# Performance work log

Measured on AMD Instinct MI355X. Metric: run time of the kernel, lower is better.

The kernel has to match this reference:

```python
import jax, jax.numpy as jnp
import numpy as np

RATE = 0.999  # moving_average_rate
EPS_NORM = 1e-12
EPS_CNT = 1e-6


def l2norm(v, axis=-1):
    # matches torch F.normalize(dim=axis) with default eps
    n = jnp.sqrt(jnp.sum(v * v, axis=axis, keepdims=True))
    return v / jnp.maximum(n, EPS_NORM)


def setup_inputs() -> dict:
    key = jax.random.key(0)
    ks = jax.random.split(key, 7)
    b, c, h, w, k = 8, 256, 64, 64, 2048
    x = jax.random.normal(ks[0], (b, c, h, w), dtype=jnp.float32)
    y = jax.random.uniform(ks[1], (b, 4, h, w), dtype=jnp.float32)
    feat_w = jax.random.normal(ks[2], (k, c + 4), dtype=jnp.float32) * 0.02
    w1 = jax.random.normal(ks[3], (c + 4, c), dtype=jnp.float32) * 0.02
    b1 = jnp.zeros((c,), dtype=jnp.float32)
    w2 = jax.random.normal(ks[4], (c, c), dtype=jnp.float32) * 0.02
    b2 = jnp.zeros((c,), dtype=jnp.float32)
    return {"x": x, "y": y, "feat_w": feat_w, "w1": w1, "b1": b1, "w2": w2, "b2": b2}


def reference(x, y, feat_w, w1, b1, w2, b2):
    b, c, h, w = x.shape
    k = feat_w.shape[0]
    # flatten spatial: (n, c) with n = b*h*w
    x_flat = jnp.transpose(x, (0, 2, 3, 1)).reshape(-1, c)
    y_flat = jnp.transpose(y, (0, 2, 3, 1)).reshape(-1, 4)

    # cosine-similarity scores against codebook features (no grad in original)
    xn = l2norm(x_flat)                       # (n, c)
    mn = l2norm(feat_w[:, :-4])               # (k, c)
    score = xn @ mn.T                         # (n, k)

    # top1 EMA codebook update
    xy = jnp.concatenate([x_flat, y_flat], axis=1)          # (n, c+4)
    ind = jnp.argmax(score, axis=1)                          # (n,)
    counts = jax.ops.segment_sum(jnp.ones_like(ind, jnp.float32), ind, num_segments=k)  # (k,)
    sums = jax.ops.segment_sum(xy, ind, num_segments=k)      # (k, c+4)
    embed_mean = sums / (counts[:, None] + EPS_CNT)          # (k, c+4)
    new_w = feat_w * RATE + embed_mean * (1.0 - RATE)        # (k, c+4)

    # softmax attention over (updated) normalized codebook
    p = jax.nn.softmax(score, axis=1)                        # (n, k)
    out = p @ l2norm(new_w)                                  # (n, c+4)

    # MLP: Linear -> GELU -> Linear (drop=0)
    out = jax.nn.gelu(out @ w1 + b1) @ w2 + b2               # (n, c)
    return jnp.transpose(out.reshape(b, h, w, c), (0, 3, 1, 2))
```

## Files before the change

kernel.cpp:

```cpp
#include <hip/hip_runtime.h>
#include <cstdint>
#include <cstddef>


typedef short v8s __attribute__((ext_vector_type(8)));
typedef float v4f __attribute__((ext_vector_type(4)));

__device__ __forceinline__ unsigned short f2b(float f) {
  unsigned u = __float_as_uint(f);
  u = (u + 0x7FFFu + ((u >> 16) & 1u)) >> 16;
  return (unsigned short)u;
}
__device__ __forceinline__ float b2f(short s) {
  return __uint_as_float((unsigned)(unsigned short)s << 16);
}
__device__ __forceinline__ float gelu_t(float x) {
  float x3 = x * x * x;
  return 0.5f * x * (1.0f + tanhf(0.7978845608028654f * (x + 0.044715f * x3)));
}
__device__ __forceinline__ float gelu_fast(float x) {
  float u = 0.7978845608028654f * (x + 0.044715f * x * x * x);
  float tt = __expf(2.0f * u);
  return x * tt * __builtin_amdgcn_rcpf(tt + 1.0f);
}
__device__ __forceinline__ unsigned int mono(float f) {
  unsigned u = __float_as_uint(f);
  return (u & 0x80000000u) ? ~u : (u | 0x80000000u);
}
__device__ __forceinline__ void async16(const short* g, short* l) {
  __builtin_amdgcn_global_load_lds(
      (const __attribute__((address_space(1))) unsigned int*)g,
      (__attribute__((address_space(3))) unsigned int*)l, 16, 0, 0);
}

__global__ void transpose_norm_kernel(const float* __restrict__ x, short* __restrict__ xn,
                                      float* __restrict__ norms) {
  __shared__ float tile[32 * 257];
  __shared__ float part[8][32];
  __shared__ float invn[32];
  int t = threadIdx.x, bx = blockIdx.x;
  int b = bx >> 7, st = bx & 127;
  int s0 = st * 32;
  int sl = t & 31, cp = t >> 5;
  const float* xb = x + (size_t)b * 256 * 4096 + s0 + sl;
  float ss = 0.f;
#pragma unroll 4
  for (int i = 0; i < 32; ++i) {
    int c = cp * 32 + i;
    float v = xb[(size_t)c * 4096];
    tile[sl * 257 + c] = v;
    ss += v * v;
  }
  part[cp][sl] = ss;
  __syncthreads();
  if (t < 32) {
    float tot = 0.f;
#pragma unroll
    for (int p = 0; p < 8; ++p) tot += part[p][t];
    float nrm = fmaxf(sqrtf(tot), 1e-12f);
    invn[t] = 1.0f / nrm;
    norms[(size_t)b * 4096 + s0 + t] = nrm;
  }
  __syncthreads();
  size_t obase = ((size_t)b * 4096 + s0) * 256 + t;
  for (int s = 0; s < 32; ++s)
    xn[obase + (size_t)s * 256] = (short)f2b(tile[s * 257 + t] * invn[s]);
}

__global__ void cbnorm_kernel(const float* __restrict__ fw, short* __restrict__ mn) {
  int t = threadIdx.x;
  int wv = t >> 6, l = t & 63;
  int r = blockIdx.x * 4 + wv;
  const float* row = fw + (size_t)r * 260;
  float v[4]; float ss = 0.f;
#pragma unroll
  for (int p = 0; p < 4; ++p) { v[p] = row[l + p * 64]; ss += v[p] * v[p]; }
#pragma unroll
  for (int m = 1; m < 64; m <<= 1) ss += __shfl_xor(ss, m, 64);
  float inv = 1.0f / fmaxf(sqrtf(ss), 1e-12f);
#pragma unroll
  for (int p = 0; p < 4; ++p) mn[(size_t)r * 256 + l + p * 64] = (short)f2b(v[p] * inv);
}

template <int KTOT, int LDA, int LDB>
__device__ __forceinline__ void gemm_core(const short* __restrict__ A, const short* __restrict__ B,
                                          int mt, int nt, int t, v4f acc[4][4],
                                          short* As, short* Bs) {
  const int l = t & 63, w = t >> 6;
  const int wm = w >> 1, wn = w & 1;
  const int lane16 = l & 15, q4 = l >> 4;
#pragma unroll
  for (int i = 0; i < 4; ++i)
#pragma unroll
    for (int j = 0; j < 4; ++j)
#pragma unroll
      for (int r = 0; r < 4; ++r) acc[i][j][r] = 0.0f;
  const int srow = (w << 5) + (l >> 2);
  const int scol = (l & 3) << 3;
  const short* ga = A + (size_t)(mt * 128 + srow) * LDA + scol;
  const short* gb = B + (size_t)(nt * 128 + srow) * LDB + scol;
  short* la = As + (w << 5) * 32;
  short* lb = Bs + (w << 5) * 32;
  for (int kk = 0; kk < KTOT; kk += 32) {
    async16(ga + kk, la);
    async16(ga + (size_t)16 * LDA + kk, la + 16 * 32);
    async16(gb + kk, lb);
    async16(gb + (size_t)16 * LDB + kk, lb + 16 * 32);
    __syncthreads();
    v8s af[4], bf[4];
#pragma unroll
    for (int i = 0; i < 4; ++i) af[i] = *(const v8s*)&As[(wm * 64 + i * 16 + lane16) * 32 + q4 * 8];
#pragma unroll
    for (int j = 0; j < 4; ++j) bf[j] = *(const v8s*)&Bs[(wn * 64 + j * 16 + lane16) * 32 + q4 * 8];
#pragma unroll
    for (int i = 0; i < 4; ++i)
#pragma unroll
      for (int j = 0; j < 4; ++j)
        acc[i][j] = __builtin_amdgcn_mfma_f32_16x16x32_bf16(af[i], bf[j], acc[i][j], 0, 0, 0);
    __syncthreads();
  }
}

__global__ __launch_bounds__(256, 2) void gemm1_kernel(const short* __restrict__ A, const short* __restrict__ B,
                                                       short* __restrict__ Q,
                                                       unsigned long long* __restrict__ packed,
                                                       float* __restrict__ lrow) {
  __shared__ __align__(16) short As[128 * 32];
  __shared__ __align__(16) short Bs[128 * 32];
  int t = threadIdx.x, bx = blockIdx.x;
  int mt = bx >> 4, nt = bx & 15;
  v4f acc[4][4];
  gemm_core<256, 256, 256>(A, B, mt, nt, t, acc, As, Bs);
  int l = t & 63, w = t >> 6, wm = w >> 1, wn = w & 1, lane16 = l & 15, q4 = l >> 4;
  int rowbase = mt * 128 + wm * 64, colbase = nt * 128 + wn * 64;
#pragma unroll
  for (int i = 0; i < 4; ++i) {
#pragma unroll
    for (int r = 0; r < 4; ++r) {
      int row_g = rowbase + i * 16 + q4 * 4 + r;
      float qs = 0.f;
      unsigned long long best = 0ull;
#pragma unroll
      for (int j = 0; j < 4; ++j) {
        float s = acc[i][j][r];
        int col_g = colbase + j * 16 + lane16;
        float qv = __expf(s) - 1.0f;
        Q[(size_t)row_g * 2048 + col_g] = (short)f2b(qv);
        qs += qv;
        unsigned long long key = ((unsigned long long)mono(s) << 32) |
                                 (unsigned long long)(unsigned int)(~(unsigned)col_g);
        if (key > best) best = key;
      }
#pragma unroll
      for (int m = 1; m < 16; m <<= 1) {
        unsigned long long ob = __shfl_xor(best, m, 64);
        if (ob > best) best = ob;
        qs += __shfl_xor(qs, m, 64);
      }
      if (lane16 == 0) {
        atomicMax(&packed[row_g], best);
        atomicAdd(&lrow[row_g], qs);
      }
    }
  }
}

__global__ void ind_kernel(const unsigned long long* __restrict__ packed,
                           int* __restrict__ ind, float* __restrict__ cnt) {
  int i = blockIdx.x * 256 + threadIdx.x;
  unsigned int lowbits = (unsigned int)(packed[i] & 0xFFFFFFFFull);
  int id = (int)(~lowbits);
  ind[i] = id;
  atomicAdd(&cnt[id], 1.0f);
}

__global__ void scan_kernel(const float* __restrict__ cnt, int* __restrict__ offs,
                            int* __restrict__ cursor) {
  __shared__ int part[256];
  int t = threadIdx.x;
  int local[8]; int s = 0;
#pragma unroll
  for (int i = 0; i < 8; ++i) { local[i] = s; s += (int)cnt[t * 8 + i]; }
  part[t] = s;
  __syncthreads();
  for (int off = 1; off < 256; off <<= 1) {
    int v = (t >= off) ? part[t - off] : 0;
    __syncthreads();
    part[t] += v;
    __syncthreads();
  }
  int base = (t > 0) ? part[t - 1] : 0;
#pragma unroll
  for (int i = 0; i < 8; ++i) {
    int o = base + local[i];
    offs[t * 8 + i] = o;
    cursor[t * 8 + i] = o;
  }
  if (t == 255) offs[2048] = part[255];
}

__global__ void fill_kernel(const int* __restrict__ ind, int* __restrict__ cursor,
                            int* __restrict__ sorted) {
  int i = blockIdx.x * 256 + threadIdx.x;
  int id = ind[i];
  int pos = atomicAdd(&cursor[id], 1);
  sorted[pos] = i;
}

__global__ void segsum_kernel(const short* __restrict__ xn, const float* __restrict__ norms,
                              const float* __restrict__ y, const int* __restrict__ offs,
                              const int* __restrict__ sorted, float* __restrict__ sums) {
  int r = blockIdx.x, t = threadIdx.x;
  int beg = offs[r], end = offs[r + 1];
  float a0 = 0.f, a1 = 0.f;
  for (int j = beg; j < end; ++j) {
    int node = sorted[j];
    float nm = norms[node];
    a0 += b2f(xn[(size_t)node * 256 + t]) * nm;
    if (t < 4) {
      int b = node >> 12, s = node & 4095;
      a1 += y[(size_t)b * 16384 + t * 4096 + s];
    }
  }
  sums[(size_t)r * 260 + t] = a0;
  if (t < 4) sums[(size_t)r * 260 + 256 + t] = a1;
}

__global__ void neww_kernel(const float* __restrict__ fw, const float* __restrict__ sums,
                            const float* __restrict__ cnt, short* __restrict__ nwt,
                            float* __restrict__ colsum) {
  int r = blockIdx.x;
  int l = threadIdx.x;
  float cv = cnt[r] + 1e-6f;
  float vals[5]; float ss = 0.f;
#pragma unroll
  for (int p = 0; p < 5; ++p) {
    int c = l + p * 64;
    float v = 0.f;
    if (c < 260) {
      float m = sums[(size_t)r * 260 + c] / cv;
      v = fw[(size_t)r * 260 + c] * 0.999f + m * 0.001f;
    }
    vals[p] = v; ss += v * v;
  }
#pragma unroll
  for (int m = 1; m < 64; m <<= 1) ss += __shfl_xor(ss, m, 64);
  float inv = 1.0f / fmaxf(sqrtf(ss), 1e-12f);
#pragma unroll
  for (int p = 0; p < 5; ++p) {
    int c = l + p * 64;
    if (c < 260) {
      float v = vals[p] * inv;
      nwt[(size_t)c * 2048 + r] = (short)f2b(v);
      atomicAdd(&colsum[c], v);
    }
  }
}

__global__ void const_kernel(const float* __restrict__ colsum, const float* __restrict__ w1,
                             const float* __restrict__ b1, const float* __restrict__ w2,
                             const float* __restrict__ b2, float* __restrict__ c0,
                             float* __restrict__ zc, float* __restrict__ hc,
                             float* __restrict__ oc) {
  __shared__ float c0s[260], hcs[256];
  int t = threadIdx.x;
  for (int c = t; c < 260; c += 256) {
    float v = colsum[c] * (1.0f / 2048.0f);
    c0s[c] = v; c0[c] = v;
  }
  __syncthreads();
  float z = b1[t];
  for (int i = 0; i < 260; ++i) z = fmaf(c0s[i], w1[(size_t)i * 256 + t], z);
  float h = gelu_t(z);
  zc[t] = z; hc[t] = h; hcs[t] = h;
  __syncthreads();
  float o = b2[t];
  for (int i = 0; i < 256; ++i) o = fmaf(hcs[i], w2[(size_t)i * 256 + t], o);
  oc[t] = o;
}

__global__ void wtrans_kernel(const float* __restrict__ w1, const float* __restrict__ w2,
                              short* __restrict__ w1t, short* __restrict__ w2t) {
  int j = blockIdx.x;
  int t = threadIdx.x;
  if (j < 256) {
    for (int i = t; i < 288; i += 64)
      w1t[(size_t)j * 288 + i] = (short)f2b(i < 260 ? w1[(size_t)i * 256 + j] : 0.0f);
  } else {
    int jj = j - 256;
    for (int i = t; i < 256; i += 64)
      w2t[(size_t)jj * 256 + i] = (short)f2b(w2[(size_t)i * 256 + jj]);
  }
}

__global__ __launch_bounds__(256, 2) void gemm2_kernel(const short* __restrict__ A, const short* __restrict__ B,
                                                       const float* __restrict__ lrow,
                                                       const float* __restrict__ colsum,
                                                       const float* __restrict__ c0,
                                                       short* __restrict__ D) {
  __shared__ __align__(16) short As[128 * 32];
  __shared__ __align__(16) short Bs[128 * 32];
  int t = threadIdx.x, bx = blockIdx.x;
  int mt = bx / 3, nt = bx % 3;
  v4f acc[4][4];
  gemm_core<2048, 2048, 2048>(A, B, mt, nt, t, acc, As, Bs);
  int l = t & 63, w = t >> 6, wm = w >> 1, wn = w & 1, lane16 = l & 15, q4 = l >> 4;
  int rowbase = mt * 128 + wm * 64, colbase = nt * 128 + wn * 64;
#pragma unroll
  for (int i = 0; i < 4; ++i) {
#pragma unroll
    for (int r = 0; r < 4; ++r) {
      int row_g = rowbase + i * 16 + q4 * 4 + r;
      float linv = 1.0f / (2048.0f + lrow[row_g]);
#pragma unroll
      for (int j = 0; j < 4; ++j) {
        int col_g = colbase + j * 16 + lane16;
        if (col_g < 288) {
          float v = 0.0f;
          if (col_g < 260) {
            float attn = (colsum[col_g] + acc[i][j][r]) * linv;
            v = attn - c0[col_g];
          }
          D[(size_t)row_g * 288 + col_g] = (short)f2b(v);
        }
      }
    }
  }
}

__global__ __launch_bounds__(256, 2) void gemm3_kernel(const short* __restrict__ A, const short* __restrict__ B,
                                                       const float* __restrict__ zc,
                                                       const float* __restrict__ hc,
                                                       short* __restrict__ E) {
  __shared__ __align__(16) short As[128 * 32];
  __shared__ __align__(16) short Bs[128 * 32];
  int t = threadIdx.x, bx = blockIdx.x;
  int mt = bx >> 1, nt = bx & 1;
  v4f acc[4][4];
  gemm_core<288, 288, 288>(A, B, mt, nt, t, acc, As, Bs);
  int l = t & 63, w = t >> 6, wm = w >> 1, wn = w & 1, lane16 = l & 15, q4 = l >> 4;
  int rowbase = mt * 128 + wm * 64, colbase = nt * 128 + wn * 64;
#pragma unroll
  for (int i = 0; i < 4; ++i)
#pragma unroll
    for (int r = 0; r < 4; ++r) {
      int row_g = rowbase + i * 16 + q4 * 4 + r;
#pragma unroll
      for (int j = 0; j < 4; ++j) {
        int col_g = colbase + j * 16 + lane16;
        float z = zc[col_g] + acc[i][j][r];
        E[(size_t)row_g * 256 + col_g] = (short)f2b(gelu_fast(z) - hc[col_g]);
      }
    }
}

__global__ __launch_bounds__(256, 2) void gemm4_kernel(const short* __restrict__ A, const short* __restrict__ B,
                                                       const float* __restrict__ oc,
                                                       float* __restrict__ T) {
  __shared__ __align__(16) short As[128 * 32];
  __shared__ __align__(16) short Bs[128 * 32];
  int t = threadIdx.x, bx = blockIdx.x;
  int mt = bx >> 1, nt = bx & 1;
  v4f acc[4][4];
  gemm_core<256, 256, 256>(A, B, mt, nt, t, acc, As, Bs);
  int l = t & 63, w = t >> 6, wm = w >> 1, wn = w & 1, lane16 = l & 15, q4 = l >> 4;
  int rowbase = mt * 128 + wm * 64, colbase = nt * 128 + wn * 64;
#pragma unroll
  for (int i = 0; i < 4; ++i)
#pragma unroll
    for (int r = 0; r < 4; ++r) {
      int row_g = rowbase + i * 16 + q4 * 4 + r;
#pragma unroll
      for (int j = 0; j < 4; ++j) {
        int col_g = colbase + j * 16 + lane16;
        T[(size_t)row_g * 256 + col_g] = oc[col_g] + acc[i][j][r];
      }
    }
}

__global__ void outtrans_kernel(const float* __restrict__ tmp, float* __restrict__ out) {
  __shared__ float tl[64 * 65];
  int bx = blockIdx.x;
  int ct = bx & 3, rt = bx >> 2;
  int r0 = rt * 64, c0 = ct * 64;
  int t = threadIdx.x;
  int tr = t >> 6, tc = t & 63;
#pragma unroll
  for (int i = 0; i < 16; ++i) {
    int rr = tr + i * 4;
    tl[rr * 65 + tc] = tmp[(size_t)(r0 + rr) * 256 + c0 + tc];
  }
  __syncthreads();
  int b = r0 >> 12, sb = r0 & 4095;
#pragma unroll
  for (int i = 0; i < 16; ++i) {
    int ccl = tr + i * 4;
    out[(size_t)b * 1048576 + (size_t)(c0 + ccl) * 4096 + sb + tc] = tl[tc * 65 + ccl];
  }
}

extern "C" void kernel_launch(void* const* d_in, const int* in_sizes, int n_in,
                              void* d_out, int out_size, void* d_ws, size_t ws_size,
                              hipStream_t stream) {
  const float* x  = (const float*)d_in[0];
  const float* y  = (const float*)d_in[1];
  const float* fw = (const float*)d_in[2];
  const float* w1 = (const float*)d_in[3];
  const float* b1 = (const float*)d_in[4];
  const float* w2 = (const float*)d_in[5];
  const float* b2 = (const float*)d_in[6];
  float* out = (float*)d_out;
  char* ws = (char*)d_ws;

  short* qbuf = (short*)(ws + 0);
  float* tmpo = (float*)(ws + 0);
  short* xn   = (short*)(ws + 134217728);
  short* ebuf = xn;
  short* mn   = (short*)(ws + 150994944);
  unsigned long long* packed = (unsigned long long*)(ws + 152043520);
  float* lrow = (float*)(ws + 152305664);
  int*   ind  = (int*)(ws + 152436736);
  float* cnt  = (float*)(ws + 152567808);
  float* sums = (float*)(ws + 152576000);
  short* nwt  = (short*)(ws + 154705920);
  float* colsum = (float*)(ws + 156278784);
  float* c0   = (float*)(ws + 156279936);
  float* zc   = (float*)(ws + 156281088);
  float* hc   = (float*)(ws + 156282112);
  float* oc   = (float*)(ws + 156283136);
  short* w1t  = (short*)(ws + 156284160);
  short* w2t  = (short*)(ws + 156431616);
  short* dbuf = (short*)(ws + 156562688);
  float* norms  = (float*)(ws + 156562688);
  int*   offs   = (int*)(ws + 156693760);
  int*   cursor = (int*)(ws + 156702464);
  int*   sorted = (int*)(ws + 156710656);
  if (ws_size < 175437056ull) return;

  hipMemsetAsync(packed, 0, 262144, stream);
  hipMemsetAsync(lrow,   0, 131072, stream);
  hipMemsetAsync(cnt,    0, 8192, stream);
  hipMemsetAsync(nwt,    0, 1572864, stream);
  hipMemsetAsync(colsum, 0, 1152, stream);

  transpose_norm_kernel<<<1024, 256, 0, stream>>>(x, xn, norms);
  cbnorm_kernel<<<512, 256, 0, stream>>>(fw, mn);
  gemm1_kernel<<<4096, 256, 0, stream>>>(xn, mn, qbuf, packed, lrow);
  ind_kernel<<<128, 256, 0, stream>>>(packed, ind, cnt);
  scan_kernel<<<1, 256, 0, stream>>>(cnt, offs, cursor);
  fill_kernel<<<128, 256, 0, stream>>>(ind, cursor, sorted);
  segsum_kernel<<<2048, 256, 0, stream>>>(xn, norms, y, offs, sorted, sums);
  neww_kernel<<<2048, 64, 0, stream>>>(fw, sums, cnt, nwt, colsum);
  const_kernel<<<1, 256, 0, stream>>>(colsum, w1, b1, w2, b2, c0, zc, hc, oc);
  wtrans_kernel<<<512, 64, 0, stream>>>(w1, w2, w1t, w2t);
  gemm2_kernel<<<768, 256, 0, stream>>>(qbuf, nwt, lrow, colsum, c0, dbuf);
  gemm3_kernel<<<512, 256, 0, stream>>>(dbuf, w1t, zc, hc, ebuf);
  gemm4_kernel<<<512, 256, 0, stream>>>(ebuf, w2t, oc, tmpo);
  outtrans_kernel<<<2048, 256, 0, stream>>>(tmpo, out);
}
```

Measured before the change: 440.4 us.

## Stage GEMM epilogues through shared memory and fuse output transpose into gemm4

Each GEMM epilogue now writes its tile into LDS in two halves and then stores to global memory with 16-byte vector writes, replacing the scattered 2-byte per-lane stores. gemm4 transposes its tile through LDS and writes straight into the NCHW output, which removes the fp32 temp buffer and the separate outtrans kernel. Launch bounds go up to 4 blocks per CU. The extra barriers and serialized half-tile passes add synchronization, and the higher occupancy target may limit registers.

```diff
diff --git a/kernel.cpp b/kernel.cpp
--- a/kernel.cpp
+++ b/kernel.cpp
@@ -121,46 +121,61 @@
   }
 }
 
-__global__ __launch_bounds__(256, 2) void gemm1_kernel(const short* __restrict__ A, const short* __restrict__ B,
+__global__ __launch_bounds__(256, 4) void gemm1_kernel(const short* __restrict__ A, const short* __restrict__ B,
                                                        short* __restrict__ Q,
                                                        unsigned long long* __restrict__ packed,
                                                        float* __restrict__ lrow) {
-  __shared__ __align__(16) short As[128 * 32];
-  __shared__ __align__(16) short Bs[128 * 32];
+  __shared__ __align__(16) short smem[8704];
+  short* As = smem;
+  short* Bs = smem + 4096;
   int t = threadIdx.x, bx = blockIdx.x;
   int mt = bx >> 4, nt = bx & 15;
   v4f acc[4][4];
   gemm_core<256, 256, 256>(A, B, mt, nt, t, acc, As, Bs);
   int l = t & 63, w = t >> 6, wm = w >> 1, wn = w & 1, lane16 = l & 15, q4 = l >> 4;
-  int rowbase = mt * 128 + wm * 64, colbase = nt * 128 + wn * 64;
-#pragma unroll
-  for (int i = 0; i < 4; ++i) {
-#pragma unroll
-    for (int r = 0; r < 4; ++r) {
-      int row_g = rowbase + i * 16 + q4 * 4 + r;
-      float qs = 0.f;
-      unsigned long long best = 0ull;
-#pragma unroll
-      for (int j = 0; j < 4; ++j) {
-        float s = acc[i][j][r];
-        int col_g = colbase + j * 16 + lane16;
-        float qv = __expf(s) - 1.0f;
-        Q[(size_t)row_g * 2048 + col_g] = (short)f2b(qv);
-        qs += qv;
-        unsigned long long key = ((unsigned long long)mono(s) << 32) |
-                                 (unsigned long long)(unsigned int)(~(unsigned)col_g);
-        if (key > best) best = key;
+  int rowbase = mt * 128, colbase = nt * 128;
+  for (int p = 0; p < 2; ++p) {
+    __syncthreads();
+    if (wm == p) {
+#pragma unroll
+      for (int i = 0; i < 4; ++i) {
+#pragma unroll
+        for (int r = 0; r < 4; ++r) {
+          int lr = i * 16 + q4 * 4 + r;
+          int row_g = rowbase + p * 64 + lr;
+          float qs = 0.f;
+          unsigned long long best = 0ull;
+#pragma unroll
+          for (int j = 0; j < 4; ++j) {
+            float s = acc[i][j][r];
+            int col_l = wn * 64 + j * 16 + lane16;
+            float qv = __expf(s) - 1.0f;
+            smem[lr * 128 + col_l] = (short)f2b(qv);
+            qs += qv;
+            unsigned long long key = ((unsigned long long)mono(s) << 32) |
+                                     (unsigned long long)(unsigned int)(~(unsigned)(colbase + col_l));
+            if (key > best) best = key;
+          }
+#pragma unroll
+          for (int m = 1; m < 16; m <<= 1) {
+            unsigned long long ob = __shfl_xor(best, m, 64);
+            if (ob > best) best = ob;
+            qs += __shfl_xor(qs, m, 64);
+          }
+          if (lane16 == 0) {
+            atomicMax(&packed[row_g], best);
+            atomicAdd(&lrow[row_g], qs);
+          }
+        }
       }
-#pragma unroll
-      for (int m = 1; m < 16; m <<= 1) {
-        unsigned long long ob = __shfl_xor(best, m, 64);
-        if (ob > best) best = ob;
-        qs += __shfl_xor(qs, m, 64);
-      }
-      if (lane16 == 0) {
-        atomicMax(&packed[row_g], best);
-        atomicAdd(&lrow[row_g], qs);
-      }
+    }
+    __syncthreads();
+#pragma unroll
+    for (int k2 = 0; k2 < 4; ++k2) {
+      int idx = k2 * 256 + t;
+      int row = idx >> 4, c8 = (idx & 15) * 8;
+      *(v8s*)&Q[(size_t)(rowbase + p * 64 + row) * 2048 + colbase + c8] =
+          *(const v8s*)&smem[row * 128 + c8];
     }
   }
 }
@@ -293,109 +308,136 @@
   }
 }
 
-__global__ __launch_bounds__(256, 2) void gemm2_kernel(const short* __restrict__ A, const short* __restrict__ B,
+__global__ __launch_bounds__(256, 4) void gemm2_kernel(const short* __restrict__ A, const short* __restrict__ B,
                                                        const float* __restrict__ lrow,
                                                        const float* __restrict__ colsum,
                                                        const float* __restrict__ c0,
                                                        short* __restrict__ D) {
-  __shared__ __align__(16) short As[128 * 32];
-  __shared__ __align__(16) short Bs[128 * 32];
+  __shared__ __align__(16) short smem[8704];
+  short* As = smem;
+  short* Bs = smem + 4096;
   int t = threadIdx.x, bx = blockIdx.x;
   int mt = bx / 3, nt = bx % 3;
   v4f acc[4][4];
   gemm_core<2048, 2048, 2048>(A, B, mt, nt, t, acc, As, Bs);
   int l = t & 63, w = t >> 6, wm = w >> 1, wn = w & 1, lane16 = l & 15, q4 = l >> 4;
-  int rowbase = mt * 128 + wm * 64, colbase = nt * 128 + wn * 64;
-#pragma unroll
-  for (int i = 0; i < 4; ++i) {
-#pragma unroll
-    for (int r = 0; r < 4; ++r) {
-      int row_g = rowbase + i * 16 + q4 * 4 + r;
-      float linv = 1.0f / (2048.0f + lrow[row_g]);
-#pragma unroll
-      for (int j = 0; j < 4; ++j) {
-        int col_g = colbase + j * 16 + lane16;
-        if (col_g < 288) {
-          float v = 0.0f;
-          if (col_g < 260) {
-            float attn = (colsum[col_g] + acc[i][j][r]) * linv;
-            v = attn - c0[col_g];
+  int rowbase = mt * 128, colbase = nt * 128;
+  for (int p = 0; p < 2; ++p) {
+    __syncthreads();
+    if (wm == p) {
+#pragma unroll
+      for (int i = 0; i < 4; ++i) {
+#pragma unroll
+        for (int r = 0; r < 4; ++r) {
+          int lr = i * 16 + q4 * 4 + r;
+          int row_g = rowbase + p * 64 + lr;
+          float linv = 1.0f / (2048.0f + lrow[row_g]);
+#pragma unroll
+          for (int j = 0; j < 4; ++j) {
+            int col_l = wn * 64 + j * 16 + lane16;
+            int col_g = colbase + col_l;
+            float v = 0.0f;
+            if (col_g < 260)
+              v = (colsum[col_g] + acc[i][j][r]) * linv - c0[col_g];
+            smem[lr * 128 + col_l] = (short)f2b(v);
           }
-          D[(size_t)row_g * 288 + col_g] = (short)f2b(v);
         }
       }
     }
-  }
-}
-
-__global__ __launch_bounds__(256, 2) void gemm3_kernel(const short* __restrict__ A, const short* __restrict__ B,
+    __syncthreads();
+#pragma unroll
+    for (int k2 = 0; k2 < 4; ++k2) {
+      int idx = k2 * 256 + t;
+      int row = idx >> 4, c8 = (idx & 15) * 8;
+      int cc = colbase + c8;
+      if (cc < 288)
+        *(v8s*)&D[(size_t)(rowbase + p * 64 + row) * 288 + cc] =
+            *(const v8s*)&smem[row * 128 + c8];
+    }
+  }
+}
+
+__global__ __launch_bounds__(256, 4) void gemm3_kernel(const short* __restrict__ A, const short* __restrict__ B,
                                                        const float* __restrict__ zc,
                                                        const float* __restrict__ hc,
                                                        short* __restrict__ E) {
-  __shared__ __align__(16) short As[128 * 32];
-  __shared__ __align__(16) short Bs[128 * 32];
+  __shared__ __align__(16) short smem[8704];
+  short* As = smem;
+  short* Bs = smem + 4096;
   int t = threadIdx.x, bx = blockIdx.x;
   int mt = bx >> 1, nt = bx & 1;
   v4f acc[4][4];
   gemm_core<288, 288, 288>(A, B, mt, nt, t, acc, As, Bs);
   int l = t & 63, w = t >> 6, wm = w >> 1, wn = w & 1, lane16 = l & 15, q4 = l >> 4;
-  int rowbase = mt * 128 + wm * 64, colbase = nt * 128 + wn * 64;
-#pragma unroll
-  for (int i = 0; i < 4; ++i)
-#pragma unroll
-    for (int r = 0; r < 4; ++r) {
-      int row_g = rowbase + i * 16 + q4 * 4 + r;
-#pragma unroll
-      for (int j = 0; j < 4; ++j) {
-        int col_g = colbase + j * 16 + lane16;
-        float z = zc[col_g] + acc[i][j][r];
-        E[(size_t)row_g * 256 + col_g] = (short)f2b(gelu_fast(z) - hc[col_g]);
-      }
-    }
-}
-
-__global__ __launch_bounds__(256, 2) void gemm4_kernel(const short* __restrict__ A, const short* __restrict__ B,
+  int rowbase = mt * 128, colbase = nt * 128;
+  for (int p = 0; p < 2; ++p) {
+    __syncthreads();
+    if (wm == p) {
+#pragma unroll
+      for (int i = 0; i < 4; ++i)
+#pragma unroll
+        for (int r = 0; r < 4; ++r) {
+          int lr = i * 16 + q4 * 4 + r;
+#pragma unroll
+          for (int j = 0; j < 4; ++j) {
+            int col_l = wn * 64 + j * 16 + lane16;
+            int col_g = colbase + col_l;
+            float z = zc[col_g] + acc[i][j][r];
+            smem[lr * 128 + col_l] = (short)f2b(gelu_fast(z) - hc[col_g]);
+          }
+        }
+    }
+    __syncthreads();
+#pragma unroll
+    for (int k2 = 0; k2 < 4; ++k2) {
+      int idx = k2 * 256 + t;
+      int row = idx >> 4, c8 = (idx & 15) * 8;
+      *(v8s*)&E[(size_t)(rowbase + p * 64 + row) * 256 + colbase + c8] =
+          *(const v8s*)&smem[row * 128 + c8];
+    }
+  }
+}
+
+__global__ __launch_bounds__(256, 4) void gemm4_kernel(const short* __restrict__ A, const short* __restrict__ B,
                                                        const float* __restrict__ oc,
-                                                       float* __restrict__ T) {
-  __shared__ __align__(16) short As[128 * 32];
-  __shared__ __align__(16) short Bs[128 * 32];
+                                                       float* __restrict__ out) {
+  __shared__ __align__(16) short smem[8704];
+  short* As = smem;
+  short* Bs = smem + 4096;
+  float* F = (float*)smem;
   int t = threadIdx.x, bx = blockIdx.x;
   int mt = bx >> 1, nt = bx & 1;
   v4f acc[4][4];
   gemm_core<256, 256, 256>(A, B, mt, nt, t, acc, As, Bs);
   int l = t & 63, w = t >> 6, wm = w >> 1, wn = w & 1, lane16 = l & 15, q4 = l >> 4;
-  int rowbase = mt * 128 + wm * 64, colbase = nt * 128 + wn * 64;
-#pragma unroll
-  for (int i = 0; i < 4; ++i)
-#pragma unroll
-    for (int r = 0; r < 4; ++r) {
-      int row_g = rowbase + i * 16 + q4 * 4 + r;
-#pragma unroll
-      for (int j = 0; j < 4; ++j) {
-        int col_g = colbase + j * 16 + lane16;
-        T[(size_t)row_g * 256 + col_g] = oc[col_g] + acc[i][j][r];
-      }
-    }
-}
-
-__global__ void outtrans_kernel(const float* __restrict__ tmp, float* __restrict__ out) {
-  __shared__ float tl[64 * 65];
-  int bx = blockIdx.x;
-  int ct = bx & 3, rt = bx >> 2;
-  int r0 = rt * 64, c0 = ct * 64;
-  int t = threadIdx.x;
-  int tr = t >> 6, tc = t & 63;
-#pragma unroll
-  for (int i = 0; i < 16; ++i) {
-    int rr = tr + i * 4;
-    tl[rr * 65 + tc] = tmp[(size_t)(r0 + rr) * 256 + c0 + tc];
-  }
-  __syncthreads();
-  int b = r0 >> 12, sb = r0 & 4095;
-#pragma unroll
-  for (int i = 0; i < 16; ++i) {
-    int ccl = tr + i * 4;
-    out[(size_t)b * 1048576 + (size_t)(c0 + ccl) * 4096 + sb + tc] = tl[tc * 65 + ccl];
+  int b_ = mt >> 5;
+  int sbase = (mt & 31) * 128;
+  for (int q = 0; q < 4; ++q) {
+    __syncthreads();
+    if (wn == (q >> 1)) {
+#pragma unroll
+      for (int i = 0; i < 4; ++i)
+#pragma unroll
+        for (int r = 0; r < 4; ++r) {
+          int srow = wm * 64 + i * 16 + q4 * 4 + r;
+#pragma unroll
+          for (int jj = 0; jj < 2; ++jj) {
+            int j = (q & 1) * 2 + jj;
+            int c_in = jj * 16 + lane16;
+            int col_g = nt * 128 + q * 32 + c_in;
+            F[c_in * 132 + srow] = oc[col_g] + acc[i][j][r];
+          }
+        }
+    }
+    __syncthreads();
+#pragma unroll
+    for (int k2 = 0; k2 < 4; ++k2) {
+      int idx = k2 * 256 + t;
+      int c_loc = idx >> 5, s4 = (idx & 31) * 4;
+      v4f vv = *(const v4f*)&F[c_loc * 132 + s4];
+      int cg = nt * 128 + q * 32 + c_loc;
+      *(v4f*)&out[(size_t)b_ * 1048576 + (size_t)cg * 4096 + sbase + s4] = vv;
+    }
   }
 }
 
@@ -413,7 +455,6 @@
   char* ws = (char*)d_ws;
 
   short* qbuf = (short*)(ws + 0);
-  float* tmpo = (float*)(ws + 0);
   short* xn   = (short*)(ws + 134217728);
   short* ebuf = xn;
   short* mn   = (short*)(ws + 150994944);
@@ -455,6 +496,5 @@
   wtrans_kernel<<<512, 64, 0, stream>>>(w1, w2, w1t, w2t);
   gemm2_kernel<<<768, 256, 0, stream>>>(qbuf, nwt, lrow, colsum, c0, dbuf);
   gemm3_kernel<<<512, 256, 0, stream>>>(dbuf, w1t, zc, hc, ebuf);
-  gemm4_kernel<<<512, 256, 0, stream>>>(ebuf, w2t, oc, tmpo);
-  outtrans_kernel<<<2048, 256, 0, stream>>>(tmpo, out);
-}
+  gemm4_kernel<<<512, 256, 0, stream>>>(ebuf, w2t, oc, out);
+}
```

Result: slower. 517.4 us (+17.5%).
